# Optimization experiments

Hardware: AMD Instinct MI355X
Metric: run time of the kernel (lower is better)

Reference implementation:

```python
import jax, jax.numpy as jnp
import numpy as np

EPS = 1e-12  # torch F.normalize eps

def _l2norm(x):
    n = jnp.sqrt(jnp.sum(x * x, axis=-1, keepdims=True))
    return x / jnp.maximum(n, EPS)

def setup_inputs() -> dict:
    key = jax.random.key(0)
    k1, k2 = jax.random.split(key)
    B, C, H, W = 4, 256, 48, 48
    qkv = jax.random.normal(k1, (B, 3 * C, H, W), dtype=jnp.float32)
    temp = jnp.ones((8, 1, 1), dtype=jnp.float32)
    proj_w = jax.random.normal(k2, (C, C), dtype=jnp.float32) * (1.0 / np.sqrt(C))
    proj_b = jnp.zeros((C,), dtype=jnp.float32)
    return {"qkv": qkv, "temp": temp, "proj_w": proj_w, "proj_b": proj_b, "h": H, "w": W}

def reference(qkv, temp, proj_w, proj_b, h, w):
    num_heads = temp.shape[0]
    b = qkv.shape[0]
    q, k, v = jnp.split(qkv, 3, axis=1)

    def to_heads(x):
        # b (head c) h w -> b head (h w) c
        return x.reshape(b, num_heads, -1, h * w).transpose(0, 1, 3, 2)

    q = _l2norm(to_heads(q))
    k = _l2norm(to_heads(k))
    v = to_heads(v)

    # [b, head, N, N], temp (head,1,1) broadcasts over (n, m)
    attn = jnp.einsum('bhnc,bhmc->bhnm', q, k) * temp
    attn = jax.nn.softmax(jax.nn.relu(attn), axis=-1)
    out = jnp.einsum('bhnm,bhmc->bhnc', attn, v)
    # b head N c -> b head c N -> b (head c) h w
    out = out.transpose(0, 1, 3, 2).reshape(b, -1, h, w)
    # 1x1 conv == channel matmul
    out = jnp.einsum('oc,bchw->bohw', proj_w, out) + proj_b[None, :, None, None]
    return out
```

## Files before the change

### kernel.cpp

```cpp
#include <hip/hip_runtime.h>

typedef unsigned short u16;
typedef unsigned int   u32;
typedef __attribute__((ext_vector_type(8))) short short8;
typedef __attribute__((ext_vector_type(4))) float f32x4;

#define NB    4
#define NCH   256
#define NHD   8
#define HD    32
#define NSP   2304
#define NBH   32
#define NKT   36
#define KPW   9

__device__ __forceinline__ u16 f2bf(float f) {
    u32 u = __float_as_uint(f);
    u += 0x7FFFu + ((u >> 16) & 1u);
    return (u16)(u >> 16);
}
__device__ __forceinline__ u32 pack2(float a, float b) {
    return (u32)f2bf(a) | ((u32)f2bf(b) << 16);
}
__device__ __forceinline__ u32 pkfast(float a, float b) {
#if __has_builtin(__builtin_amdgcn_cvt_pk_bf16_f32)
    typedef __attribute__((ext_vector_type(2))) __bf16 bf2;
    union { bf2 v; u32 u; } cv;
    cv.v = __builtin_amdgcn_cvt_pk_bf16_f32(a, b);
    return cv.u;
#else
    return __builtin_amdgcn_perm(__float_as_uint(b), __float_as_uint(a), 0x07060302u);
#endif
}
__device__ __forceinline__ float fexp2(float x) {
#if __has_builtin(__builtin_amdgcn_exp2f)
    return __builtin_amdgcn_exp2f(x);
#else
    return exp2f(x);
#endif
}

__global__ __launch_bounds__(256) void wcast_kernel(const float* __restrict__ w,
                                                    u16* __restrict__ wb) {
    int i = blockIdx.x * 256 + threadIdx.x;
    float4 v = ((const float4*)w)[i];
    ((uint2*)wb)[i] = make_uint2(pack2(v.x, v.y), pack2(v.z, v.w));
}

__global__ __launch_bounds__(64) void prep_kernel(
    const float* __restrict__ qkv, const float* __restrict__ temp,
    u16* __restrict__ Qn, u16* __restrict__ Kn, u16* __restrict__ Vp)
{
    const int p  = blockIdx.y;
    const int bh = blockIdx.z, b = bh >> 3, head = bh & 7;
    const int n  = blockIdx.x * 64 + threadIdx.x;
    const float* src = qkv + ((size_t)(b * 3 * NCH + p * NCH + head * HD)) * NSP + n;

    float v[HD];
#pragma unroll
    for (int d = 0; d < HD; ++d) v[d] = src[(size_t)d * NSP];

    if (p == 2) {
        const int loc = threadIdx.x, c = loc >> 5, r5 = loc & 31;
        const int qd  = (r5 < 16) ? (r5 >> 2) : ((r5 - 16) >> 2);
        const int jj  = (r5 < 16) ? (r5 & 3) : (4 + (r5 & 3));
        u16* dst = Vp + (size_t)bh * NSP * HD + (size_t)blockIdx.x * 2048 + c * 32 + qd * 8 + jj;
#pragma unroll
        for (int d = 0; d < HD; ++d) dst[d * 64] = f2bf(v[d]);
    } else {
        float s = 0.f;
#pragma unroll
        for (int d = 0; d < HD; ++d) s += v[d] * v[d];
        float sc = 1.f / fmaxf(sqrtf(s), 1e-12f);
        if (p == 0) sc *= temp[head] * 1.44269504088896f;
        u32 pk[HD / 2];
#pragma unroll
        for (int i = 0; i < HD / 2; ++i) pk[i] = pack2(v[2 * i] * sc, v[2 * i + 1] * sc);
        u16* dst = (p == 0 ? Qn : Kn) + ((size_t)bh * NSP + n) * HD;
#pragma unroll
        for (int i = 0; i < 4; ++i) ((uint4*)dst)[i] = ((const uint4*)pk)[i];
    }
}

__global__ __launch_bounds__(256, 4) void attn_kernel(
    const u16* __restrict__ Qn, const u16* __restrict__ Kn,
    const u16* __restrict__ Vp, u16* __restrict__ X)
{
    __shared__ float cmb[3][64][25];
    const int bh = blockIdx.x, b = bh >> 3, head = bh & 7;
    const int w = threadIdx.x >> 6, lane = threadIdx.x & 63;
    const int l15 = lane & 15, quad = lane >> 4;
    const int qbase = blockIdx.y * 32;

    const u16* Kg = Kn + (size_t)bh * NSP * HD + (size_t)w * KPW * 2048 + l15 * HD + quad * 8;
    const u16* Vg = Vp + (size_t)bh * NSP * HD + (size_t)w * KPW * 2048 + l15 * 64 + quad * 8;

    short8 qfrag[2];
#pragma unroll
    for (int t2 = 0; t2 < 2; ++t2)
        qfrag[t2] = *(const short8*)(Qn + ((size_t)bh * NSP + qbase + t2 * 16 + l15) * HD + quad * 8);

    const short one = (short)0x3F80;
    const short8 vones = {one, one, one, one, one, one, one, one};

    f32x4 oacc[2][2] = {{{0,0,0,0},{0,0,0,0}},{{0,0,0,0},{0,0,0,0}}};
    f32x4 rsac[2]    = {{0,0,0,0},{0,0,0,0}};

    short8 ka[4], vb[2][2];
#pragma unroll
    for (int i = 0; i < 4; ++i) ka[i] = *(const short8*)(Kg + i * 512);
#pragma unroll
    for (int c = 0; c < 2; ++c)
#pragma unroll
        for (int h = 0; h < 2; ++h) vb[c][h] = *(const short8*)(Vg + h * 1024 + c * 32);

    for (int kt = 0; kt < KPW; ++kt) {
        short8 kan[4], vbn[2][2];
        if (kt + 1 < KPW) {
            const u16* Kp2 = Kg + (size_t)(kt + 1) * 2048;
            const u16* Vp2 = Vg + (size_t)(kt + 1) * 2048;
#pragma unroll
            for (int i = 0; i < 4; ++i) kan[i] = *(const short8*)(Kp2 + i * 512);
#pragma unroll
            for (int c = 0; c < 2; ++c)
#pragma unroll
                for (int h = 0; h < 2; ++h) vbn[c][h] = *(const short8*)(Vp2 + h * 1024 + c * 32);
        }

#pragma unroll
        for (int t2 = 0; t2 < 2; ++t2) {
            f32x4 sf[4];
#pragma unroll
            for (int i = 0; i < 4; ++i)
                sf[i] = __builtin_amdgcn_mfma_f32_16x16x32_bf16(ka[i], qfrag[t2], (f32x4){0.f,0.f,0.f,0.f}, 0, 0, 0);
            u32 pk[4][2];
#pragma unroll
            for (int i = 0; i < 4; ++i) {
                pk[i][0] = pkfast(fexp2(fmaxf(sf[i][0], 0.f)), fexp2(fmaxf(sf[i][1], 0.f)));
                pk[i][1] = pkfast(fexp2(fmaxf(sf[i][2], 0.f)), fexp2(fmaxf(sf[i][3], 0.f)));
            }
#pragma unroll
            for (int c = 0; c < 2; ++c) {
                union { short8 s; u32 u[4]; } pa;
                pa.u[0] = pk[2 * c][0];     pa.u[1] = pk[2 * c][1];
                pa.u[2] = pk[2 * c + 1][0]; pa.u[3] = pk[2 * c + 1][1];
                oacc[t2][0] = __builtin_amdgcn_mfma_f32_16x16x32_bf16(pa.s, vb[c][0], oacc[t2][0], 0, 0, 0);
                oacc[t2][1] = __builtin_amdgcn_mfma_f32_16x16x32_bf16(pa.s, vb[c][1], oacc[t2][1], 0, 0, 0);
                rsac[t2]    = __builtin_amdgcn_mfma_f32_16x16x32_bf16(pa.s, vones,    rsac[t2],    0, 0, 0);
            }
        }

        if (kt + 1 < KPW) {
#pragma unroll
            for (int i = 0; i < 4; ++i) ka[i] = kan[i];
#pragma unroll
            for (int c = 0; c < 2; ++c)
#pragma unroll
                for (int h = 0; h < 2; ++h) vb[c][h] = vbn[c][h];
        }
    }

    if (w != 0) {
        float* dst = &cmb[w - 1][lane][0];
#pragma unroll
        for (int t2 = 0; t2 < 2; ++t2) {
#pragma unroll
            for (int h = 0; h < 2; ++h)
#pragma unroll
                for (int r = 0; r < 4; ++r) dst[t2 * 8 + h * 4 + r] = oacc[t2][h][r];
#pragma unroll
            for (int r = 0; r < 4; ++r) dst[16 + t2 * 4 + r] = rsac[t2][r];
        }
    }
    __syncthreads();
    if (w == 0) {
        u16* Xb = X + (size_t)b * NSP * NCH + head * HD;
#pragma unroll
        for (int t2 = 0; t2 < 2; ++t2) {
            float o0[4], o1[4], rsum[4];
#pragma unroll
            for (int r = 0; r < 4; ++r) {
                o0[r] = oacc[t2][0][r]; o1[r] = oacc[t2][1][r]; rsum[r] = rsac[t2][r];
            }
#pragma unroll
            for (int j = 0; j < 3; ++j) {
                const float* srcp = &cmb[j][lane][0];
#pragma unroll
                for (int r = 0; r < 4; ++r) {
                    o0[r]   += srcp[t2 * 8 + r];
                    o1[r]   += srcp[t2 * 8 + 4 + r];
                    rsum[r] += srcp[16 + t2 * 4 + r];
                }
            }
#pragma unroll
            for (int r = 0; r < 4; ++r) {
                const float inv = 1.f / rsum[r];
                u16* row = Xb + (size_t)(qbase + t2 * 16 + quad * 4 + r) * NCH;
                row[l15]      = f2bf(o0[r] * inv);
                row[16 + l15] = f2bf(o1[r] * inv);
            }
        }
    }
}

__global__ __launch_bounds__(64) void proj_kernel(
    const u16* __restrict__ Wb, const u16* __restrict__ X,
    const float* __restrict__ bias, float* __restrict__ out)
{
    const int b = blockIdx.z;
    const int lane = threadIdx.x;
    const int l15 = lane & 15, quad = lane >> 4;
    const int obase = blockIdx.y * 16;
    const int nbase = blockIdx.x * 32;

    const u16* wrow = Wb + (size_t)(obase + l15) * NCH + quad * 8;
    const u16* xrow = X + ((size_t)b * NSP + nbase + l15) * NCH + quad * 8;

    f32x4 acc[2] = {{0,0,0,0},{0,0,0,0}};
#pragma unroll
    for (int ks = 0; ks < 8; ++ks) {
        const short8 af = *(const short8*)(wrow + ks * 32);
        acc[0] = __builtin_amdgcn_mfma_f32_16x16x32_bf16(af, *(const short8*)(xrow + ks * 32), acc[0], 0, 0, 0);
        acc[1] = __builtin_amdgcn_mfma_f32_16x16x32_bf16(af, *(const short8*)(xrow + (size_t)16 * NCH + ks * 32), acc[1], 0, 0, 0);
    }
#pragma unroll
    for (int r = 0; r < 4; ++r) {
        const int o = obase + quad * 4 + r;
        const float bo = bias[o];
        float* orow = out + ((size_t)b * NCH + o) * NSP + nbase;
        orow[l15]      = acc[0][r] + bo;
        orow[16 + l15] = acc[1][r] + bo;
    }
}

extern "C" void kernel_launch(void* const* d_in, const int* in_sizes, int n_in,
                              void* d_out, int out_size, void* d_ws, size_t ws_size,
                              hipStream_t stream) {
    const float* qkv   = (const float*)d_in[0];
    const float* temp  = (const float*)d_in[1];
    const float* projw = (const float*)d_in[2];
    const float* projb = (const float*)d_in[3];
    float* out = (float*)d_out;

    u16* Qn = (u16*)d_ws;
    u16* Kn = Qn + (size_t)NBH * NSP * HD;
    u16* Vp = Kn + (size_t)NBH * NSP * HD;
    u16* X  = Vp + (size_t)NBH * NSP * HD;
    u16* Wb = X + (size_t)NB * NSP * NCH;

    wcast_kernel<<<dim3(64), dim3(256), 0, stream>>>(projw, Wb);
    prep_kernel<<<dim3(NSP / 64, 3, NBH), dim3(64), 0, stream>>>(qkv, temp, Qn, Kn, Vp);
    attn_kernel<<<dim3(NBH, NSP / 32), dim3(256), 0, stream>>>(Qn, Kn, Vp, X);
    proj_kernel<<<dim3(NSP / 32, NCH / 16, NB), dim3(64), 0, stream>>>(Wb, X, projb, out);
}
```

Measured before the change: 159.3 us.

## Double query tile per attention block, fold weight cast into prep kernel

The attention kernel now handles 64 queries per block instead of 32, so each K/V tile a wave loads is reused across four query fragments. This halves the number of blocks and the repeated K/V traffic. The cross-wave reduction now spreads the final sum and normalisation across all four waves, one query fragment each, instead of only wave 0. The separate weight-cast launch is merged into the prep kernel as an extra grid slice, and prep now uses 256-thread blocks. In exchange, V prefetch is no longer double-buffered, the occupancy hint is dropped, and register use rises, which may lower occupancy.

```diff
diff --git a/kernel.cpp b/kernel.cpp
--- a/kernel.cpp
+++ b/kernel.cpp
@@ -40,20 +40,25 @@
 #endif
 }
 
-__global__ __launch_bounds__(256) void wcast_kernel(const float* __restrict__ w,
-                                                    u16* __restrict__ wb) {
-    int i = blockIdx.x * 256 + threadIdx.x;
-    float4 v = ((const float4*)w)[i];
-    ((uint2*)wb)[i] = make_uint2(pack2(v.x, v.y), pack2(v.z, v.w));
-}
-
-__global__ __launch_bounds__(64) void prep_kernel(
+__global__ __launch_bounds__(256) void prep_kernel(
     const float* __restrict__ qkv, const float* __restrict__ temp,
-    u16* __restrict__ Qn, u16* __restrict__ Kn, u16* __restrict__ Vp)
+    const float* __restrict__ projw,
+    u16* __restrict__ Qn, u16* __restrict__ Kn, u16* __restrict__ Vp,
+    u16* __restrict__ Wb)
 {
     const int p  = blockIdx.y;
     const int bh = blockIdx.z, b = bh >> 3, head = bh & 7;
-    const int n  = blockIdx.x * 64 + threadIdx.x;
+
+    if (p == 3) {
+        const int idx = (bh * (NSP / 256) + blockIdx.x) * 256 + threadIdx.x;
+        if (idx < NCH * NCH / 4) {
+            float4 v = ((const float4*)projw)[idx];
+            ((uint2*)Wb)[idx] = make_uint2(pack2(v.x, v.y), pack2(v.z, v.w));
+        }
+        return;
+    }
+
+    const int n = blockIdx.x * 256 + threadIdx.x;
     const float* src = qkv + ((size_t)(b * 3 * NCH + p * NCH + head * HD)) * NSP + n;
 
     float v[HD];
@@ -61,10 +66,11 @@
     for (int d = 0; d < HD; ++d) v[d] = src[(size_t)d * NSP];
 
     if (p == 2) {
-        const int loc = threadIdx.x, c = loc >> 5, r5 = loc & 31;
+        const int tile = n >> 6, loc = n & 63;
+        const int c = loc >> 5, r5 = loc & 31;
         const int qd  = (r5 < 16) ? (r5 >> 2) : ((r5 - 16) >> 2);
         const int jj  = (r5 < 16) ? (r5 & 3) : (4 + (r5 & 3));
-        u16* dst = Vp + (size_t)bh * NSP * HD + (size_t)blockIdx.x * 2048 + c * 32 + qd * 8 + jj;
+        u16* dst = Vp + (size_t)bh * NSP * HD + (size_t)tile * 2048 + c * 32 + qd * 8 + jj;
 #pragma unroll
         for (int d = 0; d < HD; ++d) dst[d * 64] = f2bf(v[d]);
     } else {
@@ -82,57 +88,55 @@
     }
 }
 
-__global__ __launch_bounds__(256, 4) void attn_kernel(
+__global__ __launch_bounds__(256) void attn_kernel(
     const u16* __restrict__ Qn, const u16* __restrict__ Kn,
     const u16* __restrict__ Vp, u16* __restrict__ X)
 {
-    __shared__ float cmb[3][64][25];
+    __shared__ float cmb[4][64][49];
     const int bh = blockIdx.x, b = bh >> 3, head = bh & 7;
     const int w = threadIdx.x >> 6, lane = threadIdx.x & 63;
     const int l15 = lane & 15, quad = lane >> 4;
-    const int qbase = blockIdx.y * 32;
+    const int qbase = blockIdx.y * 64;
 
     const u16* Kg = Kn + (size_t)bh * NSP * HD + (size_t)w * KPW * 2048 + l15 * HD + quad * 8;
     const u16* Vg = Vp + (size_t)bh * NSP * HD + (size_t)w * KPW * 2048 + l15 * 64 + quad * 8;
 
-    short8 qfrag[2];
-#pragma unroll
-    for (int t2 = 0; t2 < 2; ++t2)
-        qfrag[t2] = *(const short8*)(Qn + ((size_t)bh * NSP + qbase + t2 * 16 + l15) * HD + quad * 8);
+    short8 qf[4];
+#pragma unroll
+    for (int t2 = 0; t2 < 4; ++t2)
+        qf[t2] = *(const short8*)(Qn + ((size_t)bh * NSP + qbase + t2 * 16 + l15) * HD + quad * 8);
 
     const short one = (short)0x3F80;
     const short8 vones = {one, one, one, one, one, one, one, one};
 
-    f32x4 oacc[2][2] = {{{0,0,0,0},{0,0,0,0}},{{0,0,0,0},{0,0,0,0}}};
-    f32x4 rsac[2]    = {{0,0,0,0},{0,0,0,0}};
-
-    short8 ka[4], vb[2][2];
+    f32x4 oacc[4][2] = {{{0,0,0,0},{0,0,0,0}},{{0,0,0,0},{0,0,0,0}},
+                        {{0,0,0,0},{0,0,0,0}},{{0,0,0,0},{0,0,0,0}}};
+    f32x4 rsac[4]    = {{0,0,0,0},{0,0,0,0},{0,0,0,0},{0,0,0,0}};
+
+    short8 ka[4];
 #pragma unroll
     for (int i = 0; i < 4; ++i) ka[i] = *(const short8*)(Kg + i * 512);
-#pragma unroll
-    for (int c = 0; c < 2; ++c)
-#pragma unroll
-        for (int h = 0; h < 2; ++h) vb[c][h] = *(const short8*)(Vg + h * 1024 + c * 32);
 
     for (int kt = 0; kt < KPW; ++kt) {
-        short8 kan[4], vbn[2][2];
+        short8 vb[2][2];
+#pragma unroll
+        for (int c = 0; c < 2; ++c)
+#pragma unroll
+            for (int h = 0; h < 2; ++h)
+                vb[c][h] = *(const short8*)(Vg + (size_t)kt * 2048 + h * 1024 + c * 32);
+        short8 kan[4];
         if (kt + 1 < KPW) {
             const u16* Kp2 = Kg + (size_t)(kt + 1) * 2048;
-            const u16* Vp2 = Vg + (size_t)(kt + 1) * 2048;
 #pragma unroll
             for (int i = 0; i < 4; ++i) kan[i] = *(const short8*)(Kp2 + i * 512);
-#pragma unroll
-            for (int c = 0; c < 2; ++c)
-#pragma unroll
-                for (int h = 0; h < 2; ++h) vbn[c][h] = *(const short8*)(Vp2 + h * 1024 + c * 32);
-        }
-
-#pragma unroll
-        for (int t2 = 0; t2 < 2; ++t2) {
+        }
+
+#pragma unroll
+        for (int t2 = 0; t2 < 4; ++t2) {
             f32x4 sf[4];
 #pragma unroll
             for (int i = 0; i < 4; ++i)
-                sf[i] = __builtin_amdgcn_mfma_f32_16x16x32_bf16(ka[i], qfrag[t2], (f32x4){0.f,0.f,0.f,0.f}, 0, 0, 0);
+                sf[i] = __builtin_amdgcn_mfma_f32_16x16x32_bf16(ka[i], qf[t2], (f32x4){0.f,0.f,0.f,0.f}, 0, 0, 0);
             u32 pk[4][2];
 #pragma unroll
             for (int i = 0; i < 4; ++i) {
@@ -153,52 +157,42 @@
         if (kt + 1 < KPW) {
 #pragma unroll
             for (int i = 0; i < 4; ++i) ka[i] = kan[i];
-#pragma unroll
-            for (int c = 0; c < 2; ++c)
-#pragma unroll
-                for (int h = 0; h < 2; ++h) vb[c][h] = vbn[c][h];
-        }
-    }
-
-    if (w != 0) {
-        float* dst = &cmb[w - 1][lane][0];
-#pragma unroll
-        for (int t2 = 0; t2 < 2; ++t2) {
+        }
+    }
+
+    {
+        float* my = &cmb[w][lane][0];
+#pragma unroll
+        for (int t2 = 0; t2 < 4; ++t2) {
 #pragma unroll
             for (int h = 0; h < 2; ++h)
 #pragma unroll
-                for (int r = 0; r < 4; ++r) dst[t2 * 8 + h * 4 + r] = oacc[t2][h][r];
-#pragma unroll
-            for (int r = 0; r < 4; ++r) dst[16 + t2 * 4 + r] = rsac[t2][r];
+                for (int r = 0; r < 4; ++r) my[t2 * 12 + h * 4 + r] = oacc[t2][h][r];
+#pragma unroll
+            for (int r = 0; r < 4; ++r) my[t2 * 12 + 8 + r] = rsac[t2][r];
         }
     }
     __syncthreads();
-    if (w == 0) {
+    {
+        const int t2 = w;
+        float o0[4] = {0,0,0,0}, o1[4] = {0,0,0,0}, rsum[4] = {0,0,0,0};
+#pragma unroll
+        for (int j = 0; j < 4; ++j) {
+            const float* srcp = &cmb[j][lane][t2 * 12];
+#pragma unroll
+            for (int r = 0; r < 4; ++r) {
+                o0[r]   += srcp[r];
+                o1[r]   += srcp[4 + r];
+                rsum[r] += srcp[8 + r];
+            }
+        }
         u16* Xb = X + (size_t)b * NSP * NCH + head * HD;
 #pragma unroll
-        for (int t2 = 0; t2 < 2; ++t2) {
-            float o0[4], o1[4], rsum[4];
-#pragma unroll
-            for (int r = 0; r < 4; ++r) {
-                o0[r] = oacc[t2][0][r]; o1[r] = oacc[t2][1][r]; rsum[r] = rsac[t2][r];
-            }
-#pragma unroll
-            for (int j = 0; j < 3; ++j) {
-                const float* srcp = &cmb[j][lane][0];
-#pragma unroll
-                for (int r = 0; r < 4; ++r) {
-                    o0[r]   += srcp[t2 * 8 + r];
-                    o1[r]   += srcp[t2 * 8 + 4 + r];
-                    rsum[r] += srcp[16 + t2 * 4 + r];
-                }
-            }
-#pragma unroll
-            for (int r = 0; r < 4; ++r) {
-                const float inv = 1.f / rsum[r];
-                u16* row = Xb + (size_t)(qbase + t2 * 16 + quad * 4 + r) * NCH;
-                row[l15]      = f2bf(o0[r] * inv);
-                row[16 + l15] = f2bf(o1[r] * inv);
-            }
+        for (int r = 0; r < 4; ++r) {
+            const float inv = 1.f / rsum[r];
+            u16* row = Xb + (size_t)(qbase + t2 * 16 + quad * 4 + r) * NCH;
+            row[l15]      = f2bf(o0[r] * inv);
+            row[16 + l15] = f2bf(o1[r] * inv);
         }
     }
 }
@@ -248,8 +242,7 @@
     u16* X  = Vp + (size_t)NBH * NSP * HD;
     u16* Wb = X + (size_t)NB * NSP * NCH;
 
-    wcast_kernel<<<dim3(64), dim3(256), 0, stream>>>(projw, Wb);
-    prep_kernel<<<dim3(NSP / 64, 3, NBH), dim3(64), 0, stream>>>(qkv, temp, Qn, Kn, Vp);
-    attn_kernel<<<dim3(NBH, NSP / 32), dim3(256), 0, stream>>>(Qn, Kn, Vp, X);
+    prep_kernel<<<dim3(NSP / 256, 4, NBH), dim3(256), 0, stream>>>(qkv, temp, projw, Qn, Kn, Vp, Wb);
+    attn_kernel<<<dim3(NBH, NSP / 64), dim3(256), 0, stream>>>(Qn, Kn, Vp, X);
     proj_kernel<<<dim3(NSP / 32, NCH / 16, NB), dim3(64), 0, stream>>>(Wb, X, projb, out);
 }
```

Measured after the change: 147.8 us. 7.2% less time.
